# Kernel optimization log

Hardware: AMD Instinct MI355X
Metric: run time of the kernel (lower is better)

Reference implementation:

```python
import jax, jax.numpy as jnp
import numpy as np

# Model dims (rexgen/WLN canonical hyperparameters)
B, N, MAXNB, NBONDS = 16, 100, 10, 120
AF, BF, H, BIN = 82, 6, 300, 11
DEPTH, K = 3, 80


def setup_inputs() -> dict:
    key = jax.random.key(0)
    ks = jax.random.split(key, 24)
    f32 = jnp.float32
    inp = {}
    inp["fatoms"] = jax.random.normal(ks[0], (B, N, AF), f32)
    inp["fbonds"] = jax.random.normal(ks[1], (B, NBONDS, BF), f32)
    inp["atom_nb"] = jax.random.randint(ks[2], (B, N, MAXNB), 0, N)
    inp["bond_nb"] = jax.random.randint(ks[3], (B, N, MAXNB), 0, NBONDS)
    inp["num_nbs"] = jnp.full((B, N), MAXNB, jnp.int32)
    inp["n_atoms"] = jnp.full((B,), N, jnp.int32)
    inp["binary_feats"] = jax.random.normal(ks[4], (B, N, N, BIN), f32)
    inp["mask_neis"] = (jax.random.uniform(ks[5], (B, N, MAXNB, 1)) > 0.2).astype(f32)
    inp["mask_atoms"] = jnp.ones((B, N, 1), f32)
    # sparse_idx enumerates all (sample, atom_i, atom_j) pairs in row-major order
    sb = jnp.repeat(jnp.arange(B), N * N)
    si = jnp.tile(jnp.repeat(jnp.arange(N), N), B)
    sj = jnp.tile(jnp.arange(N), B * N)
    inp["sparse_idx"] = jnp.stack([sb, si, sj], axis=1).astype(jnp.int32)

    def w(k, shape):
        return jax.random.normal(k, shape, f32) * 0.1

    # WLNet params
    inp["W_atom"] = w(ks[6], (AF, H))
    inp["W_nei_atom"] = w(ks[7], (H, H))
    inp["W_nei_bond"] = w(ks[8], (BF, H))
    inp["W_self"] = w(ks[9], (H, H))
    inp["W_U2"] = w(ks[10], (H + BF, H)); inp["b_U2"] = jnp.zeros((H,), f32)
    inp["W_U1"] = w(ks[11], (2 * H, H)); inp["b_U1"] = jnp.zeros((H,), f32)
    # Attention params
    inp["W_att_local"] = w(ks[12], (H, H))
    inp["W_att_bin"] = w(ks[13], (BIN, H)); inp["b_att"] = jnp.zeros((H,), f32)
    inp["W_att_score"] = w(ks[14], (H, 1)); inp["b_att_score"] = jnp.zeros((1,), f32)
    # ReactivityScoring params
    inp["W_pl"] = w(ks[15], (H, H))
    inp["W_pg"] = w(ks[16], (H, H))
    inp["W_pb"] = w(ks[17], (BIN, H)); inp["b_p"] = jnp.zeros((H,), f32)
    inp["W_out"] = w(ks[18], (H, 1)); inp["b_out"] = jnp.zeros((1,), f32)
    return inp


def _pair_scores(fatoms, fbonds, binary_feats, mask_neis, mask_atoms,
                 W_atom, W_nei_atom, W_nei_bond, W_self, W_U2, b_U2, W_U1, b_U1,
                 W_att_local, W_att_bin, b_att, W_att_score, b_att_score,
                 W_pl, W_pg, W_pb, b_p, W_out, b_out,
                 atom_nb, bond_nb, sparse_idx):
    bidx = jnp.arange(B)[:, None, None]
    # --- WLNet graph convolution ---
    h = jax.nn.relu(fatoms @ W_atom)                       # [B,N,H]
    local = h
    for _ in range(DEPTH):
        fnei_atom = h[bidx, atom_nb]                       # [B,N,MAXNB,H]
        fnei_bond = fbonds[bidx, bond_nb]                  # [B,N,MAXNB,BF]
        h_nei = (fnei_atom @ W_nei_atom) * (fnei_bond @ W_nei_bond)
        f_nei = (h_nei * mask_neis).sum(axis=2)            # [B,N,H]
        f_self = h @ W_self
        local = f_nei * f_self * mask_atoms                # kernel output
        nei_label = jax.nn.relu(jnp.concatenate([fnei_atom, fnei_bond], -1) @ W_U2 + b_U2)
        nei_label = (nei_label * mask_neis).sum(axis=2)
        h = jax.nn.relu(jnp.concatenate([h, nei_label], -1) @ W_U1 + b_U1)
    # --- Global attention over atom pairs ---
    pair = local[:, :, None, :] + local[:, None, :, :]     # [B,N,N,H]
    att_h = jax.nn.relu(pair @ W_att_local + binary_feats @ W_att_bin + b_att)
    att_s = jax.nn.sigmoid(att_h @ W_att_score + b_att_score)  # [B,N,N,1]
    ctx = jnp.einsum('bij,bjh->bih', att_s[..., 0], local)     # [B,N,H]
    # --- Gather sparse pairs and score reactivity ---
    sb, si, sj = sparse_idx[:, 0], sparse_idx[:, 1], sparse_idx[:, 2]
    local_pair = local[sb, si] + local[sb, sj]             # [P,H]
    global_pair = ctx[sb, si] + ctx[sb, sj]                # [P,H]
    bin_pair = binary_feats[sb, si, sj]                    # [P,BIN]
    hid = jax.nn.relu(local_pair @ W_pl + global_pair @ W_pg + bin_pair @ W_pb + b_p)
    return hid @ W_out + b_out                             # [P,1]


def reference(fatoms, fbonds, atom_nb, bond_nb, num_nbs, n_atoms, binary_feats,
              mask_neis, mask_atoms, sparse_idx,
              W_atom, W_nei_atom, W_nei_bond, W_self, W_U2, b_U2, W_U1, b_U1,
              W_att_local, W_att_bin, b_att, W_att_score, b_att_score,
              W_pl, W_pg, W_pb, b_p, W_out, b_out):
    pair_scores = _pair_scores(fatoms, fbonds, binary_feats, mask_neis, mask_atoms,
                               W_atom, W_nei_atom, W_nei_bond, W_self, W_U2, b_U2, W_U1, b_U1,
                               W_att_local, W_att_bin, b_att, W_att_score, b_att_score,
                               W_pl, W_pg, W_pb, b_p, W_out, b_out,
                               atom_nb, bond_nb, sparse_idx)
    # Segmented top-k: sparse_idx rows are grouped & ordered by sample with
    # exactly N*N pairs each, so per-sample flatten == reshape to [B, N*N].
    _, topks = jax.lax.top_k(pair_scores.reshape(B, N * N), K)  # indices, matching torch.topk[1]
    return pair_scores, topks
```

## Files before the change

kernel.cpp:

```cpp
#include <hip/hip_runtime.h>
#include <hip/hip_bf16.h>
#include <math.h>

#define BB 16
#define NN 100
#define MAXNB 10
#define NBONDS 120
#define AF 82
#define BF 6
#define HH 300
#define BIN 11
#define DEPTH 3
#define KTOP 80

typedef __attribute__((ext_vector_type(8))) short short8;
typedef __attribute__((ext_vector_type(4))) float floatx4;

__device__ __forceinline__ unsigned short f2bf(float f) {
    unsigned int u = __float_as_uint(f);
    unsigned int r = (u + 0x7FFFu + ((u >> 16) & 1u)) >> 16;
    return (unsigned short)r;
}
__device__ __forceinline__ float bf2f(unsigned short h) {
    return __uint_as_float(((unsigned int)h) << 16);
}

#define O_WATOM 0
#define O_WNB   29184
#define O_U2B   38912
#define O_WNA   48640
#define O_P1    145920
#define O_P2    243200
#define O_U1A   340480
#define O_U1B   437760
#define O_WATT  535040
#define O_WPL   632320
#define O_WPG   729600

__global__ __launch_bounds__(256) void k_prep(
    const float* __restrict__ s0, const float* __restrict__ s1,
    const float* __restrict__ s2, const float* __restrict__ s3,
    const float* __restrict__ s4, const float* __restrict__ s5,
    const float* __restrict__ s6, const float* __restrict__ s7,
    const float* __restrict__ s8, const float* __restrict__ s9,
    const float* __restrict__ s10,
    unsigned short* __restrict__ WTh, unsigned short* __restrict__ WTl,
    const float* __restrict__ fatoms, const float* __restrict__ fbonds,
    unsigned short* __restrict__ fatomsbf, unsigned short* __restrict__ fbondsbf,
    const float* __restrict__ bin, unsigned short* __restrict__ BINBF,
    const float* __restrict__ Wbin0, const float* __restrict__ Wbin1,
    unsigned short* __restrict__ WBF0, unsigned short* __restrict__ WBF1)
{
    const int z = blockIdx.z;
    if (z == 11) {
        int idx = blockIdx.x * 256 + threadIdx.x;
        if (idx < 1600 * 96) {
            int r = idx / 96, c = idx - r * 96;
            float f = (c < AF) ? fatoms[r * AF + c] : 0.f;
            unsigned short hb = f2bf(f);
            fatomsbf[r * 192 + c]      = hb;
            fatomsbf[r * 192 + 96 + c] = f2bf(f - bf2f(hb));
        } else {
            int i2 = idx - 1600 * 96;
            if (i2 < 1920 * 32) {
                int r = i2 / 32, c = i2 - r * 32;
                float f = (c < BF) ? fbonds[r * BF + c] : 0.f;
                unsigned short hb = f2bf(f);
                fbondsbf[r * 64 + c]      = hb;
                fbondsbf[r * 64 + 32 + c] = f2bf(f - bf2f(hb));
            }
        }
        return;
    }
    if (z == 12) {
        const int bx = blockIdx.x;
        if (bx < 625) {
            int p = bx * 256 + threadIdx.x;
            if (p < BB * NN * NN) {
                const float* src = bin + (size_t)p * BIN;
                unsigned short tmp[16];
#pragma unroll
                for (int k = 0; k < BIN; k++) tmp[k] = f2bf(src[k]);
#pragma unroll
                for (int k = BIN; k < 16; k++) tmp[k] = 0;
                *(uint4*)(BINBF + (size_t)p * 16) = *(uint4*)tmp;
                *(uint4*)(BINBF + (size_t)p * 16 + 8) = *(uint4*)(tmp + 8);
            }
        } else if (bx < 663) {
            int zb = bx - 625;
            const float* src = (zb >= 19) ? Wbin1 : Wbin0;
            unsigned short* dst = (zb >= 19) ? WBF1 : WBF0;
            int idx = (zb % 19) * 256 + threadIdx.x;
            int jj = idx & 7;
            int koct = (idx >> 3) & 1;
            int n = (idx >> 4) & 15;
            int ch = idx >> 8;
            int k = koct * 8 + jj;
            int h = ch * 16 + n;
            float f = (k < BIN && h < 300) ? src[k * 300 + h] : 0.f;
            dst[idx] = f2bf(f);
        }
        return;
    }
    const float* src; int K, kc, off;
    switch (z) {
        case 0:  src = s0;  K = AF;  kc = 3;  off = O_WATOM; break;
        case 1:  src = s1;  K = BF;  kc = 1;  off = O_WNB;   break;
        case 2:  src = s2;  K = BF;  kc = 1;  off = O_U2B;   break;
        case 3:  src = s3;  K = HH;  kc = 10; off = O_WNA;   break;
        case 4:  src = s4;  K = HH;  kc = 10; off = O_P1;    break;
        case 5:  src = s5;  K = HH;  kc = 10; off = O_P2;    break;
        case 6:  src = s6;  K = HH;  kc = 10; off = O_U1A;   break;
        case 7:  src = s7;  K = HH;  kc = 10; off = O_U1B;   break;
        case 8:  src = s8;  K = HH;  kc = 10; off = O_WATT;  break;
        case 9:  src = s9;  K = HH;  kc = 10; off = O_WPL;   break;
        default: src = s10; K = HH;  kc = 10; off = O_WPG;   break;
    }
    const int lim = 9728 * kc;
    int i = blockIdx.x * 256 + threadIdx.x;
    if (i < lim) {
        int jj = i & 7;
        int lane = (i >> 3) & 63;
        int rem = i >> 9;
        int kci = rem % kc;
        int ct = rem / kc;
        int k = kci * 32 + (lane >> 4) * 8 + jj;
        int col = ct * 16 + (lane & 15);
        float f = (k < K && col < 300) ? src[k * 300 + col] : 0.f;
        unsigned short hb = f2bf(f);
        WTh[off + i] = hb;
        WTl[off + i] = f2bf(f - bf2f(hb));
    }
}

__device__ __forceinline__ void gemm_core(
    const unsigned short* __restrict__ A, int lda, int kc, int M,
    const unsigned short* __restrict__ wthB, const unsigned short* __restrict__ wtlB,
    float* __restrict__ C, int ldc,
    const float* __restrict__ bias,
    const float* __restrict__ Add, int ldAdd, int addOff,
    int act, unsigned short* __restrict__ Cbf,
    int row0, int gcolBase)
{
    __shared__ unsigned short sa[16 * 648];
    if (row0 >= M) return;
    const int tid = threadIdx.x;
    const int lane = tid & 63;
    const int wid = tid >> 6;
    const int sR = kc * 64 + 8;

    {
        const uint4* Ag = (const uint4*)A;
        uint4* sa4 = (uint4*)sa;
        const int q4 = kc * 8;
        const int lda4 = lda >> 3;
        const int sR4 = q4 + 1;
        for (int i = tid; i < 16 * q4; i += 256) {
            int r = i / q4, q = i - r * q4;
            sa4[r * sR4 + q] = Ag[(size_t)(row0 + r) * lda4 + q];
        }
    }
    __syncthreads();

    const int ct = blockIdx.y * 4 + wid;
    if (ct >= 19) return;

    const int m = lane & 15;
    const int rq = lane >> 4;
    const int koct8 = rq * 8;
    const unsigned short* wth = wthB + (size_t)ct * kc * 512;
    const unsigned short* wtl = wtlB + (size_t)ct * kc * 512;

    floatx4 acc = {0.f, 0.f, 0.f, 0.f};
    for (int kci = 0; kci < kc; kci++) {
        short8 ah = *(const short8*)(sa + m * sR + kci * 32 + koct8);
        short8 al = *(const short8*)(sa + m * sR + kc * 32 + kci * 32 + koct8);
        short8 wh = *(const short8*)(wth + (kci * 64 + lane) * 8);
        short8 wl = *(const short8*)(wtl + (kci * 64 + lane) * 8);
        acc = __builtin_amdgcn_mfma_f32_16x16x32_bf16(ah, wl, acc, 0, 0, 0);
        acc = __builtin_amdgcn_mfma_f32_16x16x32_bf16(al, wh, acc, 0, 0, 0);
        acc = __builtin_amdgcn_mfma_f32_16x16x32_bf16(ah, wh, acc, 0, 0, 0);
    }

    const int col = ct * 16 + m;
    if (col < 300) {
        const float bv = bias ? bias[col] : 0.f;
        const int gcol = gcolBase + col;
#pragma unroll
        for (int r = 0; r < 4; r++) {
            const int grow = row0 + rq * 4 + r;
            float v = acc[r] + bv;
            if (Add) v += Add[(size_t)grow * ldAdd + addOff + col];
            if (act) v = fmaxf(v, 0.f);
            if (C) C[(size_t)grow * ldc + gcol] = v;
            if (Cbf) {
                unsigned short hb = f2bf(v);
                Cbf[(size_t)grow * 640 + col]       = hb;
                Cbf[(size_t)grow * 640 + 320 + col] = f2bf(v - bf2f(hb));
            }
        }
    }
}

__global__ __launch_bounds__(256) void k_gemm_mfma(
    const unsigned short* __restrict__ A, int lda, int kc, int M,
    const unsigned short* __restrict__ WTh, const unsigned short* __restrict__ WTl,
    int wtStride,
    float* __restrict__ C, int ldc,
    const float* __restrict__ bias,
    const float* __restrict__ Add, int ldAdd, int addOff,
    int act, unsigned short* __restrict__ Cbf)
{
    const int widx = blockIdx.z;
    gemm_core(A, lda, kc, M,
              WTh + (size_t)widx * wtStride, WTl + (size_t)widx * wtStride,
              C, ldc, bias, Add, ldAdd, addOff, act, Cbf,
              blockIdx.x * 16, widx * 300);
}

__global__ __launch_bounds__(256) void k_gemm_first(
    const unsigned short* __restrict__ fatomsbf,
    const unsigned short* __restrict__ fbondsbf,
    const unsigned short* __restrict__ WTh, const unsigned short* __restrict__ WTl,
    unsigned short* __restrict__ hbf, float* __restrict__ FBout)
{
    const int z = blockIdx.z;
    if (z == 0) {
        gemm_core(fatomsbf, 192, 3, 1600,
                  WTh + O_WATOM, WTl + O_WATOM,
                  nullptr, 0, nullptr, nullptr, 0, 0, 1, hbf,
                  blockIdx.x * 16, 0);
    } else {
        const int w = z - 1;
        gemm_core(fbondsbf, 64, 1, 1920,
                  WTh + O_WNB + w * 9728, WTl + O_WNB + w * 9728,
                  FBout, 600, nullptr, nullptr, 0, 0, 0, nullptr,
                  blockIdx.x * 16, w * 300);
    }
}

__global__ __launch_bounds__(320, 4) void k_neighbor(
    const float* __restrict__ HW, const float* __restrict__ FB,
    const int* __restrict__ atom_nb, const int* __restrict__ bond_nb,
    const float* __restrict__ mask_neis, const float* __restrict__ mask_atoms,
    const float* __restrict__ b_U2,
    unsigned short* __restrict__ localbf, unsigned short* __restrict__ nlbf,
    int computeU1)
{
    __shared__ int   sAn[2][MAXNB];
    __shared__ int   sBd[2][MAXNB];
    __shared__ float sM[2][MAXNB];
    __shared__ float pF[2][300];
    __shared__ float pN[2][300];
    const int tx = threadIdx.x;
    const int ty = threadIdx.y;
    const int tz = threadIdx.z;
    const int bx = blockIdx.x;
    const int bn0 = ((bx & 15) * 50 + (bx >> 4)) * 2;
    const int flat = (tz * 2 + ty) * 80 + tx;

    if (flat < 20)       sAn[flat / 10][flat % 10] = atom_nb[(bn0 + flat / 10) * MAXNB + flat % 10];
    else if (flat < 40)  { int f = flat - 20; sBd[f / 10][f % 10] = bond_nb[(bn0 + f / 10) * MAXNB + f % 10]; }
    else if (flat < 60)  { int f = flat - 40; sM[f / 10][f % 10]  = mask_neis[(bn0 + f / 10) * MAXNB + f % 10]; }
    __syncthreads();

    const int bn = bn0 + ty;
    const int b = bn / NN;
    const int h4 = tx;
    const float4* HW4 = (const float4*)HW;
    const float4* FB4 = (const float4*)FB;

    float4 fnei = make_float4(0.f, 0.f, 0.f, 0.f);
    float4 nls  = fnei;
    if (tx < 75) {
        if (computeU1) {
            const float4 bu = ((const float4*)b_U2)[h4];
#pragma unroll
            for (int kk = 0; kk < 5; kk++) {
                const int k = tz * 5 + kk;
                const int an = sAn[ty][k];
                const int bd = sBd[ty][k];
                const float m = sM[ty][k];
                const float4* hr = HW4 + (size_t)(b * NN + an) * 300;
                const float4* fr = FB4 + (size_t)(b * NBONDS + bd) * 150;
                float4 ha = hr[h4];
                float4 hu = hr[150 + h4];
                float4 fa = fr[h4];
                float4 fu = fr[75 + h4];
                fnei.x = fmaf(m, ha.x * fa.x, fnei.x);
                fnei.y = fmaf(m, ha.y * fa.y, fnei.y);
                fnei.z = fmaf(m, ha.z * fa.z, fnei.z);
                fnei.w = fmaf(m, ha.w * fa.w, fnei.w);
                float ux = hu.x + fu.x + bu.x;
                float uy = hu.y + fu.y + bu.y;
                float uz = hu.z + fu.z + bu.z;
                float uw = hu.w + fu.w + bu.w;
                nls.x = fmaf(m, fmaxf(ux, 0.f), nls.x);
                nls.y = fmaf(m, fmaxf(uy, 0.f), nls.y);
                nls.z = fmaf(m, fmaxf(uz, 0.f), nls.z);
                nls.w = fmaf(m, fmaxf(uw, 0.f), nls.w);
            }
        } else {
#pragma unroll
            for (int kk = 0; kk < 5; kk++) {
                const int k = tz * 5 + kk;
                const int an = sAn[ty][k];
                const int bd = sBd[ty][k];
                const float m = sM[ty][k];
                float4 ha = HW4[(size_t)(b * NN + an) * 300 + h4];
                float4 fa = FB4[(size_t)(b * NBONDS + bd) * 150 + h4];
                fnei.x = fmaf(m, ha.x * fa.x, fnei.x);
                fnei.y = fmaf(m, ha.y * fa.y, fnei.y);
                fnei.z = fmaf(m, ha.z * fa.z, fnei.z);
                fnei.w = fmaf(m, ha.w * fa.w, fnei.w);
            }
        }
        if (tz == 1) {
            ((float4*)pF[ty])[h4] = fnei;
            if (computeU1) ((float4*)pN[ty])[h4] = nls;
        }
    }
    __syncthreads();

    if (tx < 75 && tz == 0) {
        const float4 pf = ((const float4*)pF[ty])[h4];
        fnei.x += pf.x; fnei.y += pf.y; fnei.z += pf.z; fnei.w += pf.w;

        const float ma = mask_atoms[bn];
        const float4 sf = HW4[(size_t)bn * 300 + 75 + h4];
        float lv[4];
        lv[0] = fnei.x * sf.x * ma; lv[1] = fnei.y * sf.y * ma;
        lv[2] = fnei.z * sf.z * ma; lv[3] = fnei.w * sf.w * ma;

        ushort4 lh, ll;
        unsigned short* lhp = (unsigned short*)&lh;
        unsigned short* llp = (unsigned short*)&ll;
#pragma unroll
        for (int c = 0; c < 4; c++) {
            unsigned short hb = f2bf(lv[c]);
            lhp[c] = hb; llp[c] = f2bf(lv[c] - bf2f(hb));
        }
        *(ushort4*)(localbf + (size_t)bn * 640 + h4 * 4)       = lh;
        *(ushort4*)(localbf + (size_t)bn * 640 + 320 + h4 * 4) = ll;

        if (computeU1) {
            const float4 pn = ((const float4*)pN[ty])[h4];
            float nv[4] = {nls.x + pn.x, nls.y + pn.y, nls.z + pn.z, nls.w + pn.w};
            ushort4 nh, nl2;
            unsigned short* nhp = (unsigned short*)&nh;
            unsigned short* nlp = (unsigned short*)&nl2;
#pragma unroll
            for (int c = 0; c < 4; c++) {
                unsigned short nb = f2bf(nv[c]);
                nhp[c] = nb; nlp[c] = f2bf(nv[c] - bf2f(nb));
            }
            *(ushort4*)(nlbf + (size_t)bn * 640 + h4 * 4)       = nh;
            *(ushort4*)(nlbf + (size_t)bn * 640 + 320 + h4 * 4) = nl2;
        }
    }
}

__global__ __launch_bounds__(256) void k_pair(
    const float* __restrict__ R, int ldr,
    const unsigned short* __restrict__ BINBF,
    const unsigned short* __restrict__ WBF,
    const float* __restrict__ bvec,
    const float* __restrict__ Wscore, const float* __restrict__ bscore,
    float* __restrict__ outp, int mode)
{
    __shared__ float sLi[16 * 308];
    __shared__ float sLj[16 * 308];

    const int b  = blockIdx.x;
    const int i0 = blockIdx.y * 16;
    const int j0 = blockIdx.z * 16;
    const int tid = threadIdx.x;
    const int lane = tid & 63;
    const int wid = tid >> 6;

    for (int idx = tid; idx < 16 * 308; idx += 256) {
        int r = idx / 308;
        int c = idx - r * 308;
        float vi = 0.f, vj = 0.f;
        if (c < 300) {
            if (i0 + r < NN) vi = R[(size_t)(b * NN + i0 + r) * ldr + c] + bvec[c];
            if (j0 + r < NN) vj = R[(size_t)(b * NN + j0 + r) * ldr + c];
        }
        sLi[idx] = vi;
        sLj[idx] = vj;
    }

    const int m = lane & 15;
    const int koct = lane >> 4;
    short8 afrag[4];
#pragma unroll
    for (int g = 0; g < 4; g++) {
        int ii = i0 + wid * 4 + g; if (ii > NN - 1) ii = NN - 1;
        int jj2 = j0 + m;          if (jj2 > NN - 1) jj2 = NN - 1;
        const size_t pidx = (size_t)((b * NN + ii) * NN + jj2);
        afrag[g] = *(const short8*)(BINBF + pidx * 16 + (koct & 1) * 8);
        if (koct >= 2) afrag[g] = short8{0,0,0,0,0,0,0,0};
    }
    __syncthreads();

    const int n = lane & 15;
    const int rquad = lane >> 4;
    const floatx4 zero = {0.f, 0.f, 0.f, 0.f};
    float su[4][4];
#pragma unroll
    for (int g = 0; g < 4; g++)
#pragma unroll
        for (int r = 0; r < 4; r++) su[g][r] = 0.f;

    for (int ch = 0; ch < 19; ch++) {
        const int h0 = ch * 16;
        short8 bfrag = {0,0,0,0,0,0,0,0};
        if (lane < 32)
            bfrag = *(const short8*)(WBF + ch * 256 + (n * 2 + koct) * 8);
        float wsv = 0.f;
        if (h0 + n < 300) wsv = Wscore[h0 + n];
#pragma unroll
        for (int g = 0; g < 4; g++) {
            floatx4 P = __builtin_amdgcn_mfma_f32_16x16x32_bf16(
                afrag[g], bfrag, zero, 0, 0, 0);
            const float liv = sLi[(wid * 4 + g) * 308 + h0 + n];
#pragma unroll
            for (int r = 0; r < 4; r++) {
                const float ljv = sLj[(rquad * 4 + r) * 308 + h0 + n];
                float u = P[r] + liv + ljv;
                su[g][r] = fmaf(fmaxf(u, 0.f), wsv, su[g][r]);
            }
        }
    }

    const float bs = bscore[0];
#pragma unroll
    for (int g = 0; g < 4; g++) {
#pragma unroll
        for (int r = 0; r < 4; r++) {
            float v = su[g][r];
            v += __shfl_xor(v, 1);
            v += __shfl_xor(v, 2);
            v += __shfl_xor(v, 4);
            v += __shfl_xor(v, 8);
            if (n == 0) {
                const int i = i0 + wid * 4 + g;
                const int j = j0 + rquad * 4 + r;
                if (i < NN && j < NN) {
                    float s = v + bs;
                    outp[(size_t)(b * NN + i) * NN + j] =
                        (mode == 0) ? (1.f / (1.f + expf(-s))) : s;
                }
            }
        }
    }
}

__global__ __launch_bounds__(320, 2) void k_ctx(
    const float* __restrict__ att, const float* __restrict__ LL,
    float* __restrict__ LPG)
{
    const int bx = blockIdx.x;
    const int b = bx & 15;
    const int i0 = (bx >> 4) * 4;
    const int tid = threadIdx.x;
    __shared__ float sa[4 * NN];
    for (int idx = tid; idx < 4 * NN; idx += 320) {
        int ii = idx / NN, j = idx - ii * NN;
        sa[idx] = att[(size_t)(b * NN + i0 + ii) * NN + j];
    }
    __syncthreads();
    if (tid < HH) {
        float acc0 = 0.f, acc1 = 0.f, acc2 = 0.f, acc3 = 0.f;
#pragma unroll 4
        for (int j = 0; j < NN; j++) {
            const float lv = LL[(size_t)(b * NN + j) * 900 + 600 + tid];
            acc0 = fmaf(sa[j], lv, acc0);
            acc1 = fmaf(sa[NN + j], lv, acc1);
            acc2 = fmaf(sa[2 * NN + j], lv, acc2);
            acc3 = fmaf(sa[3 * NN + j], lv, acc3);
        }
        float vals[4] = {acc0, acc1, acc2, acc3};
#pragma unroll
        for (int k = 0; k < 4; k++) {
            LPG[(size_t)(b * NN + i0 + k) * 300 + tid] =
                vals[k] + LL[(size_t)(b * NN + i0 + k) * 900 + 300 + tid];
        }
    }
}

__global__ __launch_bounds__(1024) void k_topk(
    const float* __restrict__ scores, float* __restrict__ topk_out)
{
    const int b = blockIdx.x;
    const int tid = threadIdx.x;
    const int wid = tid >> 6;
    const int lane = tid & 63;
    const float* sc = scores + (size_t)b * (NN * NN);

    __shared__ unsigned int skey[NN * NN];
    __shared__ unsigned int whist[16 * 256];
    __shared__ unsigned int hist[256];
    __shared__ unsigned int candU[KTOP];
    __shared__ int candI[KTOP];
    __shared__ int cntG;
    __shared__ int curMin;
    __shared__ unsigned int sh_pref, sh_mask;
    __shared__ int sh_kRem;
    __shared__ int sh_last;

    for (int idx = tid; idx < NN * NN; idx += 1024) {
        unsigned int u = __float_as_uint(sc[idx]);
        u = (u & 0x80000000u) ? ~u : (u | 0x80000000u);
        skey[idx] = u;
    }
    if (tid == 0) {
        sh_pref = 0u; sh_mask = 0u; sh_kRem = KTOP; cntG = 0; sh_last = -1;
    }
    __syncthreads();

    for (int pass = 0; pass < 4; pass++) {
        const int shift = 24 - 8 * pass;
        unsigned int* wh = whist + (wid << 8);
        wh[lane] = 0u; wh[lane + 64] = 0u; wh[lane + 128] = 0u; wh[lane + 192] = 0u;
        __syncthreads();
        const unsigned int pref = sh_pref, mask = sh_mask;
        for (int idx = tid; idx < NN * NN; idx += 1024) {
            unsigned int u = skey[idx];
            if ((u & mask) == pref)
                atomicAdd(&wh[(u >> shift) & 255u], 1u);
        }
        __syncthreads();
        if (tid < 256) {
            unsigned int s = 0u;
#pragma unroll
            for (int w = 0; w < 16; w++) s += whist[(w << 8) | tid];
            hist[tid] = s;
        }
        __syncthreads();
        if (wid == 0) {
            unsigned int h0 = hist[lane * 4 + 0];
            unsigned int h1 = hist[lane * 4 + 1];
            unsigned int h2 = hist[lane * 4 + 2];
            unsigned int h3 = hist[lane * 4 + 3];
            unsigned int own = h0 + h1 + h2 + h3;
            unsigned int suf = own;
#pragma unroll
            for (int off = 1; off < 64; off <<= 1) {
                unsigned int v = __shfl_down(suf, off);
                if (lane + off < 64) suf += v;
            }
            const int k = sh_kRem;
            const unsigned int above = suf - own;
            if (above < (unsigned int)k && suf >= (unsigned int)k) {
                unsigned int c = above, hb; int bsel;
                c += h3;
                if ((int)c >= k) { bsel = lane * 4 + 3; hb = h3; }
                else { c += h2;
                    if ((int)c >= k) { bsel = lane * 4 + 2; hb = h2; }
                    else { c += h1;
                        if ((int)c >= k) { bsel = lane * 4 + 1; hb = h1; }
                        else { c += h0; bsel = lane * 4; hb = h0; } } }
                sh_kRem = k - (int)(c - hb);
                sh_pref = pref | ((unsigned int)bsel << shift);
                sh_mask = mask | (0xFFu << shift);
            }
        }
        __syncthreads();
    }
    const unsigned int T = sh_pref;

    for (int idx = tid; idx < NN * NN; idx += 1024) {
        unsigned int u = skey[idx];
        if (u > T) {
            int pos = atomicAdd(&cntG, 1);
            candU[pos] = u;
            candI[pos] = idx;
        }
    }
    __syncthreads();
    const int needE = KTOP - cntG;

    for (int e = 0; e < needE; e++) {
        if (tid == 0) curMin = 0x7fffffff;
        __syncthreads();
        const int last = sh_last;
        for (int idx = tid; idx < NN * NN; idx += 1024) {
            if (skey[idx] == T && idx > last)
                atomicMin(&curMin, idx);
        }
        __syncthreads();
        if (tid == 0) {
            candU[cntG + e] = T;
            candI[cntG + e] = curMin;
            sh_last = curMin;
        }
        __syncthreads();
    }

    if (tid < KTOP) {
        const unsigned int mu = candU[tid];
        const int mi = candI[tid];
        int rank = 0;
        for (int o = 0; o < KTOP; o++) {
            unsigned int ou = candU[o];
            int oi = candI[o];
            if (ou > mu || (ou == mu && oi < mi)) rank++;
        }
        topk_out[b * KTOP + rank] = (float)mi;
    }
}

extern "C" void kernel_launch(void* const* d_in, const int* in_sizes, int n_in,
                              void* d_out, int out_size, void* d_ws, size_t ws_size,
                              hipStream_t stream) {
    const float* fatoms       = (const float*)d_in[0];
    const float* fbonds       = (const float*)d_in[1];
    const int*   atom_nb      = (const int*)d_in[2];
    const int*   bond_nb      = (const int*)d_in[3];
    const float* binary_feats = (const float*)d_in[6];
    const float* mask_neis    = (const float*)d_in[7];
    const float* mask_atoms   = (const float*)d_in[8];
    const float* W_atom       = (const float*)d_in[10];
    const float* W_nei_atom   = (const float*)d_in[11];
    const float* W_nei_bond   = (const float*)d_in[12];
    const float* W_self       = (const float*)d_in[13];
    const float* W_U2         = (const float*)d_in[14];
    const float* b_U2         = (const float*)d_in[15];
    const float* W_U1         = (const float*)d_in[16];
    const float* b_U1         = (const float*)d_in[17];
    const float* W_att_local  = (const float*)d_in[18];
    const float* W_att_bin    = (const float*)d_in[19];
    const float* b_att        = (const float*)d_in[20];
    const float* W_att_score  = (const float*)d_in[21];
    const float* b_att_score  = (const float*)d_in[22];
    const float* W_pl         = (const float*)d_in[23];
    const float* W_pg         = (const float*)d_in[24];
    const float* W_pb         = (const float*)d_in[25];
    const float* b_p          = (const float*)d_in[26];
    const float* W_out        = (const float*)d_in[27];
    const float* b_out        = (const float*)d_in[28];

    float* ws = (float*)d_ws;
    float* HW  = ws;
    float* FB  = HW + 1920000;
    float* LL  = FB + 1152000;
    float* LPG = LL + 1440000;
    float* att = LPG + 480000;
    unsigned short* S0       = (unsigned short*)(ws + 5152000);
    unsigned short* hbf      = S0;
    unsigned short* nlbf     = S0 + 1024000;
    unsigned short* localbf  = S0 + 2048000;
    unsigned short* WTh      = S0 + 3072000;
    unsigned short* WTl      = S0 + 3898880;
    unsigned short* BINBF    = S0 + 4725760;
    unsigned short* WBF_att  = S0 + 7285760;
    unsigned short* WBF_fin  = S0 + 7290624;
    unsigned short* fatomsbf = S0 + 7295488;
    unsigned short* fbondsbf = S0 + 7602688;

    float* out = (float*)d_out;
    float* topk_out = out + (size_t)BB * NN * NN;

    k_prep<<<dim3(840, 1, 13), 256, 0, stream>>>(
        W_atom, W_nei_bond, W_U2 + 300 * 300, W_nei_atom, W_self, W_U2,
        W_U1, W_U1 + 300 * 300, W_att_local, W_pl, W_pg, WTh, WTl,
        fatoms, fbonds, fatomsbf, fbondsbf,
        binary_feats, BINBF, W_att_bin, W_pb, WBF_att, WBF_fin);

    k_gemm_first<<<dim3(120, 5, 3), 256, 0, stream>>>(
        fatomsbf, fbondsbf, WTh, WTl, hbf, FB);

    for (int d = 0; d < DEPTH; d++) {
        int nW = (d == DEPTH - 1) ? 2 : 4;
        k_gemm_mfma<<<dim3(104, 5, nW), 256, 0, stream>>>(
            hbf, 640, 10, 1600, WTh + O_WNA, WTl + O_WNA, 97280,
            HW, 1200, nullptr, nullptr, 0, 0, 0, nullptr);
        k_neighbor<<<dim3(800), dim3(80, 2, 2), 0, stream>>>(
            HW, FB, atom_nb, bond_nb, mask_neis, mask_atoms, b_U2,
            localbf, nlbf, (d < DEPTH - 1) ? 1 : 0);
        if (d < DEPTH - 1) {
            k_gemm_mfma<<<dim3(104, 5, 1), 256, 0, stream>>>(
                nlbf, 640, 10, 1600, WTh + O_U1B, WTl + O_U1B, 0,
                nullptr, 0, b_U1, HW, 1200, 900, 1, hbf);
        }
    }

    k_gemm_mfma<<<dim3(104, 5, 3), 256, 0, stream>>>(
        localbf, 640, 10, 1600, WTh + O_WATT, WTl + O_WATT, 97280,
        LL, 900, nullptr, nullptr, 0, 0, 0, nullptr);

    k_pair<<<dim3(16, 7, 7), 256, 0, stream>>>(
        LL, 900, BINBF, WBF_att, b_att, W_att_score, b_att_score,
        att, 0);

    k_ctx<<<dim3(BB * 25), 320, 0, stream>>>(att, LL, LPG);

    k_pair<<<dim3(16, 7, 7), 256, 0, stream>>>(
        LPG, 300, BINBF, WBF_fin, b_p, W_out, b_out,
        out, 1);

    k_topk<<<dim3(BB), 1024, 0, stream>>>(out, topk_out);
}
```

Measured before the change: 288.2 us.

## Fuse U1 GEMM halves into one concatenated-K GEMM with ping-pong atom buffers

Before, the h@W_U1a product came out of the batched neighbor-atom GEMM as a fourth weight slice, and was added in the epilogue of a separate nl@W_U1b GEMM. Now the two U1 weight halves are packed into one K=600 weight tile, and a new kernel reads both h and nl into shared memory and computes the whole U1 update in a single GEMM. The fourth slice is dropped, so HW shrinks to three slices and the fp32 round-trip for the U1a partial disappears. The h buffer is double-buffered because the new kernel reads the old h while writing the new one.

```diff
diff --git a/kernel.cpp b/kernel.cpp
--- a/kernel.cpp
+++ b/kernel.cpp
@@ -31,8 +31,7 @@
 #define O_WNA   48640
 #define O_P1    145920
 #define O_P2    243200
-#define O_U1A   340480
-#define O_U1B   437760
+#define O_U1CAT 340480
 #define O_WATT  535040
 #define O_WPL   632320
 #define O_WPG   729600
@@ -102,7 +101,7 @@
         }
         return;
     }
-    const float* src; int K, kc, off;
+    const float* src; int K, kc, off, u1base = -1;
     switch (z) {
         case 0:  src = s0;  K = AF;  kc = 3;  off = O_WATOM; break;
         case 1:  src = s1;  K = BF;  kc = 1;  off = O_WNB;   break;
@@ -110,8 +109,8 @@
         case 3:  src = s3;  K = HH;  kc = 10; off = O_WNA;   break;
         case 4:  src = s4;  K = HH;  kc = 10; off = O_P1;    break;
         case 5:  src = s5;  K = HH;  kc = 10; off = O_P2;    break;
-        case 6:  src = s6;  K = HH;  kc = 10; off = O_U1A;   break;
-        case 7:  src = s7;  K = HH;  kc = 10; off = O_U1B;   break;
+        case 6:  src = s6;  K = HH;  kc = 10; off = O_U1CAT; u1base = 0;  break;
+        case 7:  src = s7;  K = HH;  kc = 10; off = O_U1CAT; u1base = 10; break;
         case 8:  src = s8;  K = HH;  kc = 10; off = O_WATT;  break;
         case 9:  src = s9;  K = HH;  kc = 10; off = O_WPL;   break;
         default: src = s10; K = HH;  kc = 10; off = O_WPG;   break;
@@ -128,8 +127,11 @@
         int col = ct * 16 + (lane & 15);
         float f = (k < K && col < 300) ? src[k * 300 + col] : 0.f;
         unsigned short hb = f2bf(f);
-        WTh[off + i] = hb;
-        WTl[off + i] = f2bf(f - bf2f(hb));
+        int dsti = (u1base >= 0)
+                 ? off + ct * 10240 + (kci + u1base) * 512 + lane * 8 + jj
+                 : off + i;
+        WTh[dsti] = hb;
+        WTl[dsti] = f2bf(f - bf2f(hb));
     }
 }
 
@@ -216,6 +218,71 @@
               WTh + (size_t)widx * wtStride, WTl + (size_t)widx * wtStride,
               C, ldc, bias, Add, ldAdd, addOff, act, Cbf,
               blockIdx.x * 16, widx * 300);
+}
+
+__global__ __launch_bounds__(256) void k_gemm_u1(
+    const unsigned short* __restrict__ Ah,
+    const unsigned short* __restrict__ An,
+    const unsigned short* __restrict__ WTh, const unsigned short* __restrict__ WTl,
+    const float* __restrict__ bias,
+    unsigned short* __restrict__ Cbf)
+{
+    __shared__ unsigned short sa[16 * 1288];
+    const int row0 = blockIdx.x * 16;
+    if (row0 >= 1600) return;
+    const int tid = threadIdx.x;
+    const int lane = tid & 63;
+    const int wid = tid >> 6;
+
+    {
+        const uint4* Ag = (const uint4*)Ah;
+        const uint4* Ng = (const uint4*)An;
+        uint4* sa4 = (uint4*)sa;
+        for (int i = tid; i < 16 * 160; i += 256) {
+            int r = i / 160, q = i - r * 160;
+            const size_t rb = (size_t)(row0 + r) * 80;
+            uint4 v;
+            if (q < 40)       v = Ag[rb + q];
+            else if (q < 80)  v = Ng[rb + (q - 40)];
+            else if (q < 120) v = Ag[rb + (q - 40)];
+            else              v = Ng[rb + (q - 80)];
+            sa4[r * 161 + q] = v;
+        }
+    }
+    __syncthreads();
+
+    const int ct = blockIdx.y * 4 + wid;
+    if (ct >= 19) return;
+
+    const int m = lane & 15;
+    const int rq = lane >> 4;
+    const int koct8 = rq * 8;
+    const unsigned short* wth = WTh + (size_t)ct * 10240;
+    const unsigned short* wtl = WTl + (size_t)ct * 10240;
+
+    floatx4 acc = {0.f, 0.f, 0.f, 0.f};
+    for (int kci = 0; kci < 20; kci++) {
+        short8 ah = *(const short8*)(sa + m * 1288 + kci * 32 + koct8);
+        short8 al = *(const short8*)(sa + m * 1288 + 640 + kci * 32 + koct8);
+        short8 wh = *(const short8*)(wth + (kci * 64 + lane) * 8);
+        short8 wl = *(const short8*)(wtl + (kci * 64 + lane) * 8);
+        acc = __builtin_amdgcn_mfma_f32_16x16x32_bf16(ah, wl, acc, 0, 0, 0);
+        acc = __builtin_amdgcn_mfma_f32_16x16x32_bf16(al, wh, acc, 0, 0, 0);
+        acc = __builtin_amdgcn_mfma_f32_16x16x32_bf16(ah, wh, acc, 0, 0, 0);
+    }
+
+    const int col = ct * 16 + m;
+    if (col < 300) {
+        const float bv = bias[col];
+#pragma unroll
+        for (int r = 0; r < 4; r++) {
+            const int grow = row0 + rq * 4 + r;
+            float v = fmaxf(acc[r] + bv, 0.f);
+            unsigned short hb = f2bf(v);
+            Cbf[(size_t)grow * 640 + col]       = hb;
+            Cbf[(size_t)grow * 640 + 320 + col] = f2bf(v - bf2f(hb));
+        }
+    }
 }
 
 __global__ __launch_bounds__(256) void k_gemm_first(
@@ -281,7 +348,7 @@
                 const int an = sAn[ty][k];
                 const int bd = sBd[ty][k];
                 const float m = sM[ty][k];
-                const float4* hr = HW4 + (size_t)(b * NN + an) * 300;
+                const float4* hr = HW4 + (size_t)(b * NN + an) * 225;
                 const float4* fr = FB4 + (size_t)(b * NBONDS + bd) * 150;
                 float4 ha = hr[h4];
                 float4 hu = hr[150 + h4];
@@ -307,7 +374,7 @@
                 const int an = sAn[ty][k];
                 const int bd = sBd[ty][k];
                 const float m = sM[ty][k];
-                float4 ha = HW4[(size_t)(b * NN + an) * 300 + h4];
+                float4 ha = HW4[(size_t)(b * NN + an) * 225 + h4];
                 float4 fa = FB4[(size_t)(b * NBONDS + bd) * 150 + h4];
                 fnei.x = fmaf(m, ha.x * fa.x, fnei.x);
                 fnei.y = fmaf(m, ha.y * fa.y, fnei.y);
@@ -327,7 +394,7 @@
         fnei.x += pf.x; fnei.y += pf.y; fnei.z += pf.z; fnei.w += pf.w;
 
         const float ma = mask_atoms[bn];
-        const float4 sf = HW4[(size_t)bn * 300 + 75 + h4];
+        const float4 sf = HW4[(size_t)bn * 225 + 75 + h4];
         float lv[4];
         lv[0] = fnei.x * sf.x * ma; lv[1] = fnei.y * sf.y * ma;
         lv[2] = fnei.z * sf.z * ma; lv[3] = fnei.w * sf.w * ma;
@@ -643,21 +710,22 @@
 
     float* ws = (float*)d_ws;
     float* HW  = ws;
-    float* FB  = HW + 1920000;
+    float* FB  = HW + 1440000;
     float* LL  = FB + 1152000;
     float* LPG = LL + 1440000;
     float* att = LPG + 480000;
-    unsigned short* S0       = (unsigned short*)(ws + 5152000);
+    unsigned short* S0       = (unsigned short*)(ws + 4672000);
     unsigned short* hbf      = S0;
-    unsigned short* nlbf     = S0 + 1024000;
-    unsigned short* localbf  = S0 + 2048000;
-    unsigned short* WTh      = S0 + 3072000;
-    unsigned short* WTl      = S0 + 3898880;
-    unsigned short* BINBF    = S0 + 4725760;
-    unsigned short* WBF_att  = S0 + 7285760;
-    unsigned short* WBF_fin  = S0 + 7290624;
-    unsigned short* fatomsbf = S0 + 7295488;
-    unsigned short* fbondsbf = S0 + 7602688;
+    unsigned short* hbf2     = S0 + 1024000;
+    unsigned short* nlbf     = S0 + 2048000;
+    unsigned short* localbf  = S0 + 3072000;
+    unsigned short* WTh      = S0 + 4096000;
+    unsigned short* WTl      = S0 + 4922880;
+    unsigned short* BINBF    = S0 + 5749760;
+    unsigned short* WBF_att  = S0 + 8309760;
+    unsigned short* WBF_fin  = S0 + 8314624;
+    unsigned short* fatomsbf = S0 + 8319488;
+    unsigned short* fbondsbf = S0 + 8626688;
 
     float* out = (float*)d_out;
     float* topk_out = out + (size_t)BB * NN * NN;
@@ -671,18 +739,20 @@
     k_gemm_first<<<dim3(120, 5, 3), 256, 0, stream>>>(
         fatomsbf, fbondsbf, WTh, WTl, hbf, FB);
 
+    unsigned short* hb[2] = {hbf, hbf2};
+    int cur = 0;
     for (int d = 0; d < DEPTH; d++) {
-        int nW = (d == DEPTH - 1) ? 2 : 4;
+        int nW = (d == DEPTH - 1) ? 2 : 3;
         k_gemm_mfma<<<dim3(104, 5, nW), 256, 0, stream>>>(
-            hbf, 640, 10, 1600, WTh + O_WNA, WTl + O_WNA, 97280,
-            HW, 1200, nullptr, nullptr, 0, 0, 0, nullptr);
+            hb[cur], 640, 10, 1600, WTh + O_WNA, WTl + O_WNA, 97280,
+            HW, 900, nullptr, nullptr, 0, 0, 0, nullptr);
         k_neighbor<<<dim3(800), dim3(80, 2, 2), 0, stream>>>(
             HW, FB, atom_nb, bond_nb, mask_neis, mask_atoms, b_U2,
             localbf, nlbf, (d < DEPTH - 1) ? 1 : 0);
         if (d < DEPTH - 1) {
-            k_gemm_mfma<<<dim3(104, 5, 1), 256, 0, stream>>>(
-                nlbf, 640, 10, 1600, WTh + O_U1B, WTl + O_U1B, 0,
-                nullptr, 0, b_U1, HW, 1200, 900, 1, hbf);
+            k_gemm_u1<<<dim3(104, 5, 1), 256, 0, stream>>>(
+                hb[cur], nlbf, WTh + O_U1CAT, WTl + O_U1CAT, b_U1, hb[cur ^ 1]);
+            cur ^= 1;
         }
     }
 
```

Measured after the change: 283.8 us. No clear change (-1.5%).
